# Kernel tuning notes

Hardware: AMD Instinct MI355X
Metric: run time of the kernel (lower is better)

Reference implementation:

```python
import jax, jax.numpy as jnp
import numpy as np

H, W = 512, 512
G = 8192
ALPHA_THRESH = 1.0 / 255.0        # meta_f32[0]
TRANS_THRESH = 1.0e-4             # meta_f32[1]
ALPHA_CAP = 0.99                  # meta_f32[6]
BG = jnp.zeros((3,), dtype=jnp.float32)  # config.background


def setup_inputs() -> dict:
    key = jax.random.key(0)
    ks = jax.random.split(key, 7)
    mx = jax.random.uniform(ks[0], (G,), minval=0.0, maxval=float(W))
    my = jax.random.uniform(ks[1], (G,), minval=0.0, maxval=float(H))
    means2d = jnp.stack([mx, my], axis=-1)
    # Build valid conics (inverse 2x2 covariances) from random rotation + scales
    theta = jax.random.uniform(ks[2], (G,), minval=0.0, maxval=2.0 * np.pi)
    s = jax.random.uniform(ks[3], (G, 2), minval=2.0, maxval=12.0)  # px stddevs
    ct, st = jnp.cos(theta), jnp.sin(theta)
    v1, v2 = s[:, 0] ** 2, s[:, 1] ** 2
    ca = ct * ct * v1 + st * st * v2
    cb = ct * st * (v1 - v2)
    cc = st * st * v1 + ct * ct * v2
    det = ca * cc - cb * cb
    conics = jnp.stack([cc / det, -cb / det, ca / det], axis=-1)  # [G,3] = (a,b,c)
    colors = jax.random.uniform(ks[4], (G, 3))
    opacities = jax.random.uniform(ks[5], (G,))
    depths = jax.random.uniform(ks[6], (G,), minval=0.1, maxval=100.0)
    return {"means2d": means2d, "conics": conics, "colors": colors,
            "opacities": opacities, "depths": depths}


def reference(means2d, conics, colors, opacities, depths):
    # Stable front-to-back depth sort (mirrors perm = argsort(depths, stable))
    perm = jnp.argsort(depths, stable=True)
    m = means2d[perm]
    cn = conics[perm]
    col = colors[perm]
    op = opacities[perm]
    a, b, c = cn[:, 0], cn[:, 1], cn[:, 2]
    px = jnp.arange(W, dtype=means2d.dtype) + 0.5  # pixel centers

    def row(y):
        py = y.astype(means2d.dtype) + 0.5
        dx = px[:, None] - m[None, :, 0]          # [W,G]
        dy = py - m[:, 1]                          # [G]
        sigma = 0.5 * (a * dx * dx + c * dy * dy) + b * dx * dy  # [W,G]
        alpha = jnp.minimum(ALPHA_CAP, op * jnp.exp(-sigma))
        alpha = jnp.where((sigma < 0) | (alpha < ALPHA_THRESH), 0.0, alpha)
        # exclusive cumulative transmittance along depth order
        Tprev = jnp.cumprod(1.0 - alpha, axis=-1)
        Tprev = jnp.concatenate([jnp.ones((W, 1), alpha.dtype), Tprev[:, :-1]], axis=-1)
        # early-termination: splats seen after T drops below threshold contribute 0
        wgt = alpha * Tprev * (Tprev >= TRANS_THRESH)  # [W,G]
        rgb = wgt @ col                                 # [W,3]
        t_rem = 1.0 - wgt.sum(axis=-1)                  # remaining transmittance
        return rgb + t_rem[:, None] * BG

    return jax.lax.map(row, jnp.arange(H))  # [H,W,3]
```

## Files before the change

kernel.cpp:

```cpp
#include <hip/hip_runtime.h>

#define G 8192
#define IMG_W 512
#define IMG_H 512
#define TILE 16
#define NTX (IMG_W / TILE)
#define NTY (IMG_H / TILE)
#define BLK 256
#define BLKB 64
#define CAP 1024
#define ALPHA_THRESH (1.0f/255.0f)
#define ALPHA_CAP 0.99f
#define TRANS_THRESH 1e-4f

__global__ __launch_bounds__(BLK)
void range_kernel(const float* __restrict__ means2d,
                  const float* __restrict__ conics,
                  const float* __restrict__ colors,
                  const float* __restrict__ opac,
                  unsigned int* __restrict__ ranges,
                  float* __restrict__ tbl)
{
    int g = blockIdx.x * BLK + threadIdx.x;
    if (g >= G) return;
    float op = opac[g];
    float a  = conics[3*g], b = conics[3*g+1], c = conics[3*g+2];
    float mx = means2d[2*g], my = means2d[2*g+1];
    float cr = colors[3*g], cg = colors[3*g+1], cb = colors[3*g+2];

    float4* t4 = (float4*)(tbl + (g << 4));
    t4[0] = make_float4(mx, my, 0.5f * a, b);
    t4[1] = make_float4(0.5f * c, op, cr, cg);
    t4[2] = make_float4(cb, 0.0f, 0.0f, 0.0f);

    unsigned int packed = 0xFFu;
    if (op * 255.0f >= 1.0f) {
        float smax = __logf(op * 255.0f);
        float det = fmaxf(a * c - b * b, 1e-12f);
        float rx = sqrtf(fmaxf(2.0f * smax * c / det, 0.0f)) * 1.0001f + 0.01f;
        float ry = sqrtf(fmaxf(2.0f * smax * a / det, 0.0f)) * 1.0001f + 0.01f;
        int txmin = (int)ceilf ((mx - rx - 15.5f) * 0.0625f);
        int txmax = (int)floorf((mx + rx -  0.5f) * 0.0625f);
        int tymin = (int)ceilf ((my - ry - 15.5f) * 0.0625f);
        int tymax = (int)floorf((my + ry -  0.5f) * 0.0625f);
        if (!(txmax < 0 || txmin > NTX-1 || tymax < 0 || tymin > NTY-1 ||
              txmin > txmax || tymin > tymax)) {
            txmin = max(txmin, 0); txmax = min(txmax, NTX-1);
            tymin = max(tymin, 0); tymax = min(tymax, NTY-1);
            packed = (unsigned)txmin | ((unsigned)txmax << 8)
                   | ((unsigned)tymin << 16) | ((unsigned)tymax << 24);
        }
    }
    ranges[g] = packed;
}

__device__ __forceinline__ int hitp(unsigned p, unsigned btx, unsigned bty)
{
    return (btx >= (p & 0xffu)) & (btx <= ((p >> 8) & 0xffu)) &
           (bty >= ((p >> 16) & 0xffu)) & (bty <= (p >> 24));
}

__global__ __launch_bounds__(BLK)
void tile_kernel(const unsigned int* __restrict__ ranges,
                 const float* __restrict__ depths,
                 const float* __restrict__ tbl,
                 float*       __restrict__ out)
{
    __shared__ __align__(16) unsigned short slist[CAP];
    __shared__ __align__(16) unsigned int fkeys[CAP + 8];
    __shared__ int woff[4];
    __shared__ __align__(16) float4 sq0[4][BLKB];
    __shared__ __align__(16) float4 sq1[4][BLKB];
    __shared__ __align__(16) float  sq2[4][BLKB];
    __shared__ float4 part[4][BLK];

    const int t = threadIdx.x;
    const int lane = t & 63, w = t >> 6;
    const unsigned btx = blockIdx.x, bty = blockIdx.y;

    const uint4* r4 = (const uint4*)ranges;
    const int wbase = w * (G / 4);
    uint4 rv[8];
    #pragma unroll
    for (int i = 0; i < 8; ++i)
        rv[i] = r4[(wbase >> 2) + i * 64 + lane];

    int cnt = 0;
    #pragma unroll
    for (int i = 0; i < 8; ++i)
        cnt += hitp(rv[i].x, btx, bty) + hitp(rv[i].y, btx, bty)
             + hitp(rv[i].z, btx, bty) + hitp(rv[i].w, btx, bty);
    #pragma unroll
    for (int d = 1; d < 64; d <<= 1) cnt += __shfl_xor(cnt, d);
    if (lane == 0) woff[w] = cnt;
    __syncthreads();

    int offs = 0;
    for (int ww = 0; ww < w; ++ww) offs += woff[ww];
    const int N = min(woff[0] + woff[1] + woff[2] + woff[3], CAP);

    const unsigned long long lt = (1ull << lane) - 1ull;
    #pragma unroll
    for (int i = 0; i < 8; ++i) {
        int gbase = wbase + i * 256 + lane * 4;
        int h0 = hitp(rv[i].x, btx, bty), h1 = hitp(rv[i].y, btx, bty);
        int h2 = hitp(rv[i].z, btx, bty), h3 = hitp(rv[i].w, btx, bty);
        unsigned long long m0 = __ballot(h0), m1 = __ballot(h1);
        unsigned long long m2 = __ballot(h2), m3 = __ballot(h3);
        int pos = offs + __popcll(m0 & lt) + __popcll(m1 & lt)
                       + __popcll(m2 & lt) + __popcll(m3 & lt);
        if (h0) { if (pos < CAP) slist[pos] = (unsigned short)(gbase    ); pos++; }
        if (h1) { if (pos < CAP) slist[pos] = (unsigned short)(gbase + 1); pos++; }
        if (h2) { if (pos < CAP) slist[pos] = (unsigned short)(gbase + 2); pos++; }
        if (h3) { if (pos < CAP) slist[pos] = (unsigned short)(gbase + 3); pos++; }
        offs += __popcll(m0) + __popcll(m1) + __popcll(m2) + __popcll(m3);
    }
    __syncthreads();

    unsigned short myidx[4]; unsigned int mykey[4]; int myr[4];
    #pragma unroll
    for (int m = 0; m < 4; ++m) {
        int i = t + m * BLK;
        if (i < N) {
            unsigned idx = slist[i];
            unsigned k = __float_as_uint(depths[idx]);
            myidx[m] = (unsigned short)idx; mykey[m] = k; fkeys[i] = k;
        }
    }
    if (t < 8) fkeys[N + t] = 0xFFFFFFFFu;
    __syncthreads();

    const uint4* fk4 = (const uint4*)fkeys;
    const int nj4 = (N + 3) >> 2;
    #pragma unroll
    for (int m = 0; m < 4; ++m) {
        int i = t + m * BLK;
        if (i < N) {
            unsigned ke = mykey[m]; int r = 0;
            for (int j4 = 0; j4 < nj4; ++j4) {
                uint4 kv = fk4[j4]; int j = j4 << 2;
                r += (int)((kv.x < ke) | ((kv.x == ke) & (j     < i)));
                r += (int)((kv.y < ke) | ((kv.y == ke) & (j + 1 < i)));
                r += (int)((kv.z < ke) | ((kv.z == ke) & (j + 2 < i)));
                r += (int)((kv.w < ke) | ((kv.w == ke) & (j + 3 < i)));
            }
            myr[m] = r;
        }
    }
    __syncthreads();
    #pragma unroll
    for (int m = 0; m < 4; ++m) {
        int i = t + m * BLK;
        if (i < N) slist[myr[m]] = myidx[m];
    }
    __syncthreads();

    const int csz = (N + 3) >> 2;
    const int cs = w * csz;
    const int ce = min(N, cs + csz);

    const float px  = (float)(btx * TILE + (lane & 15)) + 0.5f;
    const int   y0  = (lane >> 4) << 2;
    const float py0 = (float)(bty * TILE + y0) + 0.5f;
    const float py1 = py0 + 1.0f, py2 = py0 + 2.0f, py3 = py0 + 3.0f;

    float T0=1.f,T1=1.f,T2=1.f,T3=1.f;
    float ar0=0.f,ag0=0.f,ab0=0.f, ar1=0.f,ag1=0.f,ab1=0.f;
    float ar2=0.f,ag2=0.f,ab2=0.f, ar3=0.f,ag3=0.f,ab3=0.f;

    for (int base = cs; base < ce; base += BLKB) {
        int k = min(BLKB, ce - base);
        float4 v0 = make_float4(0.f,0.f,0.f,0.f);
        float4 v1 = make_float4(0.f,0.f,0.f,0.f);
        float  v2 = 0.f;
        if (lane < k) {
            int idx = slist[base + lane];
            const float4* b = (const float4*)(tbl + (idx << 4));
            v0 = b[0]; v1 = b[1]; v2 = ((const float*)b)[8];
        }
        sq0[w][lane] = v0; sq1[w][lane] = v1; sq2[w][lane] = v2;
        __threadfence_block();

        int k4 = (k + 3) & ~3;
        #pragma unroll 2
        for (int i = 0; i < k4; i += 4) {
            float4 blv = *(const float4*)&sq2[w][i];
            #pragma unroll
            for (int u = 0; u < 4; ++u) {
                float4 q0 = sq0[w][i + u];
                float4 q1 = sq1[w][i + u];
                float  bl = (u == 0) ? blv.x : (u == 1) ? blv.y
                          : (u == 2) ? blv.z : blv.w;
                float dx = px - q0.x;
                float dxdx = dx * dx;
                float dy0 = py0 - q0.y, dy1 = py1 - q0.y;
                float dy2 = py2 - q0.y, dy3 = py3 - q0.y;
                float sg0 = fmaf(q0.z, dxdx, fmaf(q1.x, dy0*dy0, q0.w*(dx*dy0)));
                float sg1 = fmaf(q0.z, dxdx, fmaf(q1.x, dy1*dy1, q0.w*(dx*dy1)));
                float sg2 = fmaf(q0.z, dxdx, fmaf(q1.x, dy2*dy2, q0.w*(dx*dy2)));
                float sg3 = fmaf(q0.z, dxdx, fmaf(q1.x, dy3*dy3, q0.w*(dx*dy3)));
                float al0 = q1.y * __expf(-sg0);
                float al1 = q1.y * __expf(-sg1);
                float al2 = q1.y * __expf(-sg2);
                float al3 = q1.y * __expf(-sg3);
                al0 = ((sg0 >= 0.f) && (al0 >= ALPHA_THRESH)) ? fminf(al0, ALPHA_CAP) : 0.f;
                al1 = ((sg1 >= 0.f) && (al1 >= ALPHA_THRESH)) ? fminf(al1, ALPHA_CAP) : 0.f;
                al2 = ((sg2 >= 0.f) && (al2 >= ALPHA_THRESH)) ? fminf(al2, ALPHA_CAP) : 0.f;
                al3 = ((sg3 >= 0.f) && (al3 >= ALPHA_THRESH)) ? fminf(al3, ALPHA_CAP) : 0.f;
                float w0 = al0*T0, w1 = al1*T1, w2 = al2*T2, w3 = al3*T3;
                ar0 = fmaf(w0, q1.z, ar0);  ar1 = fmaf(w1, q1.z, ar1);
                ar2 = fmaf(w2, q1.z, ar2);  ar3 = fmaf(w3, q1.z, ar3);
                ag0 = fmaf(w0, q1.w, ag0);  ag1 = fmaf(w1, q1.w, ag1);
                ag2 = fmaf(w2, q1.w, ag2);  ag3 = fmaf(w3, q1.w, ag3);
                ab0 = fmaf(w0, bl,   ab0);  ab1 = fmaf(w1, bl,   ab1);
                ab2 = fmaf(w2, bl,   ab2);  ab3 = fmaf(w3, bl,   ab3);
                T0 *= (1.f - al0);
                T1 *= (1.f - al1);
                T2 *= (1.f - al2);
                T3 *= (1.f - al3);
            }
        }
        if (__all((T0 < TRANS_THRESH) & (T1 < TRANS_THRESH) &
                  (T2 < TRANS_THRESH) & (T3 < TRANS_THRESH))) break;
    }

    {
        const int xl = lane & 15;
        part[w][(y0    ) * 16 + xl] = make_float4(ar0, ag0, ab0, T0);
        part[w][(y0 + 1) * 16 + xl] = make_float4(ar1, ag1, ab1, T1);
        part[w][(y0 + 2) * 16 + xl] = make_float4(ar2, ag2, ab2, T2);
        part[w][(y0 + 3) * 16 + xl] = make_float4(ar3, ag3, ab3, T3);
    }
    __syncthreads();

    float4 p0 = part[0][t], p1 = part[1][t], p2 = part[2][t], p3 = part[3][t];
    float r = p3.x, g = p3.y, b = p3.z;
    r = fmaf(p2.w, r, p2.x); g = fmaf(p2.w, g, p2.y); b = fmaf(p2.w, b, p2.z);
    r = fmaf(p1.w, r, p1.x); g = fmaf(p1.w, g, p1.y); b = fmaf(p1.w, b, p1.z);
    r = fmaf(p0.w, r, p0.x); g = fmaf(p0.w, g, p0.y); b = fmaf(p0.w, b, p0.z);

    const int X = (int)btx * TILE + (t & 15);
    const int Y = (int)bty * TILE + (t >> 4);
    const int o = (Y * IMG_W + X) * 3;
    out[o]     = r;
    out[o + 1] = g;
    out[o + 2] = b;
}

extern "C" void kernel_launch(void* const* d_in, const int* in_sizes, int n_in,
                              void* d_out, int out_size, void* d_ws, size_t ws_size,
                              hipStream_t stream)
{
    const float* means2d = (const float*)d_in[0];
    const float* conics  = (const float*)d_in[1];
    const float* colors  = (const float*)d_in[2];
    const float* opac    = (const float*)d_in[3];
    const float* depths  = (const float*)d_in[4];
    float* out = (float*)d_out;
    unsigned int* ranges = (unsigned int*)d_ws;
    float* tbl = (float*)((char*)d_ws + 32 * 1024);

    range_kernel<<<G / BLK, BLK, 0, stream>>>(means2d, conics, colors, opac,
                                              ranges, tbl);
    tile_kernel<<<dim3(NTX, NTY), dim3(BLK), 0, stream>>>(
        ranges, depths, tbl, out);
}
```

Measured before the change: 86.62 us.

## Cull splat-tile pairs with exact ellipse-rectangle test and per-tile bitmask

For splats whose bounding tile rectangle covers at most 32 tiles, the range kernel now tests each tile against the ellipse contour where alpha reaches the threshold, and stores a per-tile hit bitmask next to packed geometry in a uint2. Larger splats keep the plain bounding-box test. The tile kernel reads twice as much range data and decodes the mask, aiming to shrink per-tile splat lists and cut wasted exp/blend work. The sigma evaluation is also refactored into a Horner-style form that needs fewer multiplies. The trade-off is more range-kernel work, more range bytes read per tile block, and more registers for the 16 uint4 loads.

```diff
diff --git a/kernel.cpp b/kernel.cpp
--- a/kernel.cpp
+++ b/kernel.cpp
@@ -13,12 +13,44 @@
 #define ALPHA_CAP 0.99f
 #define TRANS_THRESH 1e-4f
 
+__device__ __forceinline__ bool ell_rect(float X0, float X1, float Y0, float Y1,
+                                         float a, float b, float c,
+                                         float det, float smaxt)
+{
+    if ((X0 <= 0.f) && (X1 >= 0.f) && (Y0 <= 0.f) && (Y1 >= 0.f)) return true;
+    #pragma unroll
+    for (int e = 0; e < 2; ++e) {
+        float xb = e ? X1 : X0;
+        float t = -b * xb;
+        bool lo = (t < Y0 * c);
+        bool in = !lo && (t <= Y1 * c);
+        if (in) { if (xb*xb*det <= 2.f*smaxt*c) return true; }
+        else {
+            float yc = lo ? Y0 : Y1;
+            if (0.5f*a*xb*xb + b*xb*yc + 0.5f*c*yc*yc <= smaxt) return true;
+        }
+    }
+    #pragma unroll
+    for (int e = 0; e < 2; ++e) {
+        float yb = e ? Y1 : Y0;
+        float t = -b * yb;
+        bool lo = (t < X0 * a);
+        bool in = !lo && (t <= X1 * a);
+        if (in) { if (yb*yb*det <= 2.f*smaxt*a) return true; }
+        else {
+            float xc = lo ? X0 : X1;
+            if (0.5f*a*xc*xc + b*xc*yb + 0.5f*c*yb*yb <= smaxt) return true;
+        }
+    }
+    return false;
+}
+
 __global__ __launch_bounds__(BLK)
 void range_kernel(const float* __restrict__ means2d,
                   const float* __restrict__ conics,
                   const float* __restrict__ colors,
                   const float* __restrict__ opac,
-                  unsigned int* __restrict__ ranges,
+                  uint2* __restrict__ ranges,
                   float* __restrict__ tbl)
 {
     int g = blockIdx.x * BLK + threadIdx.x;
@@ -33,7 +65,7 @@
     t4[1] = make_float4(0.5f * c, op, cr, cg);
     t4[2] = make_float4(cb, 0.0f, 0.0f, 0.0f);
 
-    unsigned int packed = 0xFFu;
+    unsigned geo = 0u, mask = 0u;
     if (op * 255.0f >= 1.0f) {
         float smax = __logf(op * 255.0f);
         float det = fmaxf(a * c - b * b, 1e-12f);
@@ -47,21 +79,48 @@
               txmin > txmax || tymin > tymax)) {
             txmin = max(txmin, 0); txmax = min(txmax, NTX-1);
             tymin = max(tymin, 0); tymax = min(tymax, NTY-1);
-            packed = (unsigned)txmin | ((unsigned)txmax << 8)
-                   | ((unsigned)tymin << 16) | ((unsigned)tymax << 24);
-        }
-    }
-    ranges[g] = packed;
-}
-
-__device__ __forceinline__ int hitp(unsigned p, unsigned btx, unsigned bty)
-{
-    return (btx >= (p & 0xffu)) & (btx <= ((p >> 8) & 0xffu)) &
-           (bty >= ((p >> 16) & 0xffu)) & (bty <= (p >> 24));
+            int wd = txmax - txmin + 1, ht = tymax - tymin + 1;
+            if (wd * ht > 32) {
+                geo = (unsigned)txmin | ((unsigned)tymin << 6)
+                    | ((unsigned)wd << 12) | ((unsigned)ht << 16) | (1u << 20);
+            } else {
+                float smaxt = smax * 1.0002f + 1e-3f;
+                unsigned m = 0u;
+                for (int tj = 0; tj < ht; ++tj) {
+                    float Y0 = (float)((tymin + tj) * TILE) + 0.5f - my - 0.01f;
+                    float Y1 = Y0 + 15.02f;
+                    for (int ti = 0; ti < wd; ++ti) {
+                        float X0 = (float)((txmin + ti) * TILE) + 0.5f - mx - 0.01f;
+                        float X1 = X0 + 15.02f;
+                        if (ell_rect(X0, X1, Y0, Y1, a, b, c, det, smaxt))
+                            m |= 1u << (tj * wd + ti);
+                    }
+                }
+                if (m) {
+                    geo = (unsigned)txmin | ((unsigned)tymin << 6)
+                        | ((unsigned)wd << 12) | ((unsigned)ht << 16);
+                    mask = m;
+                }
+            }
+        }
+    }
+    ranges[g] = make_uint2(geo, mask);
+}
+
+__device__ __forceinline__ int hitp2(unsigned geo, unsigned mask,
+                                     unsigned btx, unsigned bty)
+{
+    unsigned txm = geo & 63u, tym = (geo >> 6) & 63u;
+    unsigned wd  = (geo >> 12) & 15u, ht = (geo >> 16) & 15u;
+    unsigned dxt = btx - txm, dyt = bty - tym;
+    int inr = (dxt < wd) & (dyt < ht);
+    unsigned bi = dyt * wd + dxt;
+    int mb = (geo >> 20) ? 1 : (int)((mask >> (bi & 31u)) & 1u);
+    return inr & mb;
 }
 
 __global__ __launch_bounds__(BLK)
-void tile_kernel(const unsigned int* __restrict__ ranges,
+void tile_kernel(const uint2* __restrict__ ranges,
                  const float* __restrict__ depths,
                  const float* __restrict__ tbl,
                  float*       __restrict__ out)
@@ -80,16 +139,16 @@
 
     const uint4* r4 = (const uint4*)ranges;
     const int wbase = w * (G / 4);
-    uint4 rv[8];
-    #pragma unroll
-    for (int i = 0; i < 8; ++i)
-        rv[i] = r4[(wbase >> 2) + i * 64 + lane];
+    uint4 rv[16];
+    #pragma unroll
+    for (int i = 0; i < 16; ++i)
+        rv[i] = r4[(wbase >> 1) + i * 64 + lane];
 
     int cnt = 0;
     #pragma unroll
-    for (int i = 0; i < 8; ++i)
-        cnt += hitp(rv[i].x, btx, bty) + hitp(rv[i].y, btx, bty)
-             + hitp(rv[i].z, btx, bty) + hitp(rv[i].w, btx, bty);
+    for (int i = 0; i < 16; ++i)
+        cnt += hitp2(rv[i].x, rv[i].y, btx, bty)
+             + hitp2(rv[i].z, rv[i].w, btx, bty);
     #pragma unroll
     for (int d = 1; d < 64; d <<= 1) cnt += __shfl_xor(cnt, d);
     if (lane == 0) woff[w] = cnt;
@@ -101,19 +160,15 @@
 
     const unsigned long long lt = (1ull << lane) - 1ull;
     #pragma unroll
-    for (int i = 0; i < 8; ++i) {
-        int gbase = wbase + i * 256 + lane * 4;
-        int h0 = hitp(rv[i].x, btx, bty), h1 = hitp(rv[i].y, btx, bty);
-        int h2 = hitp(rv[i].z, btx, bty), h3 = hitp(rv[i].w, btx, bty);
+    for (int i = 0; i < 16; ++i) {
+        int gbase = wbase + i * 128 + lane * 2;
+        int h0 = hitp2(rv[i].x, rv[i].y, btx, bty);
+        int h1 = hitp2(rv[i].z, rv[i].w, btx, bty);
         unsigned long long m0 = __ballot(h0), m1 = __ballot(h1);
-        unsigned long long m2 = __ballot(h2), m3 = __ballot(h3);
-        int pos = offs + __popcll(m0 & lt) + __popcll(m1 & lt)
-                       + __popcll(m2 & lt) + __popcll(m3 & lt);
+        int pos = offs + __popcll(m0 & lt) + __popcll(m1 & lt);
         if (h0) { if (pos < CAP) slist[pos] = (unsigned short)(gbase    ); pos++; }
-        if (h1) { if (pos < CAP) slist[pos] = (unsigned short)(gbase + 1); pos++; }
-        if (h2) { if (pos < CAP) slist[pos] = (unsigned short)(gbase + 2); pos++; }
-        if (h3) { if (pos < CAP) slist[pos] = (unsigned short)(gbase + 3); pos++; }
-        offs += __popcll(m0) + __popcll(m1) + __popcll(m2) + __popcll(m3);
+        if (h1) { if (pos < CAP) slist[pos] = (unsigned short)(gbase + 1); }
+        offs += __popcll(m0) + __popcll(m1);
     }
     __syncthreads();
 
@@ -192,13 +247,14 @@
                 float  bl = (u == 0) ? blv.x : (u == 1) ? blv.y
                           : (u == 2) ? blv.z : blv.w;
                 float dx = px - q0.x;
-                float dxdx = dx * dx;
+                float A  = q0.z * (dx * dx);
+                float Bx = q0.w * dx;
                 float dy0 = py0 - q0.y, dy1 = py1 - q0.y;
                 float dy2 = py2 - q0.y, dy3 = py3 - q0.y;
-                float sg0 = fmaf(q0.z, dxdx, fmaf(q1.x, dy0*dy0, q0.w*(dx*dy0)));
-                float sg1 = fmaf(q0.z, dxdx, fmaf(q1.x, dy1*dy1, q0.w*(dx*dy1)));
-                float sg2 = fmaf(q0.z, dxdx, fmaf(q1.x, dy2*dy2, q0.w*(dx*dy2)));
-                float sg3 = fmaf(q0.z, dxdx, fmaf(q1.x, dy3*dy3, q0.w*(dx*dy3)));
+                float sg0 = fmaf(dy0, fmaf(q1.x, dy0, Bx), A);
+                float sg1 = fmaf(dy1, fmaf(q1.x, dy1, Bx), A);
+                float sg2 = fmaf(dy2, fmaf(q1.x, dy2, Bx), A);
+                float sg3 = fmaf(dy3, fmaf(q1.x, dy3, Bx), A);
                 float al0 = q1.y * __expf(-sg0);
                 float al1 = q1.y * __expf(-sg1);
                 float al2 = q1.y * __expf(-sg2);
@@ -257,8 +313,8 @@
     const float* opac    = (const float*)d_in[3];
     const float* depths  = (const float*)d_in[4];
     float* out = (float*)d_out;
-    unsigned int* ranges = (unsigned int*)d_ws;
-    float* tbl = (float*)((char*)d_ws + 32 * 1024);
+    uint2* ranges = (uint2*)d_ws;
+    float* tbl = (float*)((char*)d_ws + 64 * 1024);
 
     range_kernel<<<G / BLK, BLK, 0, stream>>>(means2d, conics, colors, opac,
                                               ranges, tbl);
```

Result: slower. 108.4 us (+25.1%).

## Split tile kernel into separate sort and single-wave compositing kernels

Applied to the files above, without the earlier changes.

Splits the fused per-tile kernel into a sort kernel, which writes each tile's depth-sorted splat list and count to workspace, and a compositing kernel launched with one 64-thread wave per tile that walks the whole list sequentially. This drops the four-wave split of the list and the shared-memory partial-transmittance merge, and gives the compositing loop a fully serial early-termination check. The cost is an extra launch, a global round trip of the sorted lists, and fewer threads per tile during compositing, which may lower latency hiding.

```diff
diff --git a/kernel.cpp b/kernel.cpp
--- a/kernel.cpp
+++ b/kernel.cpp
@@ -6,12 +6,16 @@
 #define TILE 16
 #define NTX (IMG_W / TILE)
 #define NTY (IMG_H / TILE)
+#define NTILES (NTX * NTY)
 #define BLK 256
-#define BLKB 64
 #define CAP 1024
 #define ALPHA_THRESH (1.0f/255.0f)
 #define ALPHA_CAP 0.99f
 #define TRANS_THRESH 1e-4f
+
+#define OFF_TBL   32768
+#define OFF_LIST  (OFF_TBL + G*64)
+#define OFF_N     (OFF_LIST + NTILES*CAP*2)
 
 __global__ __launch_bounds__(BLK)
 void range_kernel(const float* __restrict__ means2d,
@@ -61,22 +65,19 @@
 }
 
 __global__ __launch_bounds__(BLK)
-void tile_kernel(const unsigned int* __restrict__ ranges,
+void sort_kernel(const unsigned int* __restrict__ ranges,
                  const float* __restrict__ depths,
-                 const float* __restrict__ tbl,
-                 float*       __restrict__ out)
+                 unsigned short* __restrict__ lists,
+                 int* __restrict__ tile_n)
 {
     __shared__ __align__(16) unsigned short slist[CAP];
     __shared__ __align__(16) unsigned int fkeys[CAP + 8];
     __shared__ int woff[4];
-    __shared__ __align__(16) float4 sq0[4][BLKB];
-    __shared__ __align__(16) float4 sq1[4][BLKB];
-    __shared__ __align__(16) float  sq2[4][BLKB];
-    __shared__ float4 part[4][BLK];
 
     const int t = threadIdx.x;
     const int lane = t & 63, w = t >> 6;
     const unsigned btx = blockIdx.x, bty = blockIdx.y;
+    const int tile = (int)bty * NTX + (int)btx;
 
     const uint4* r4 = (const uint4*)ranges;
     const int wbase = w * (G / 4);
@@ -155,42 +156,54 @@
     }
     __syncthreads();
 
-    const int csz = (N + 3) >> 2;
-    const int cs = w * csz;
-    const int ce = min(N, cs + csz);
-
-    const float px  = (float)(btx * TILE + (lane & 15)) + 0.5f;
+    for (int i = t; i < N; i += BLK) lists[tile * CAP + i] = slist[i];
+    if (t == 0) tile_n[tile] = N;
+}
+
+__global__ __launch_bounds__(64)
+void comp_kernel(const unsigned short* __restrict__ lists,
+                 const int* __restrict__ tile_n,
+                 const float* __restrict__ tbl,
+                 float* __restrict__ out)
+{
+    __shared__ __align__(16) float4 sq0[64];
+    __shared__ __align__(16) float4 sq1[64];
+    __shared__ __align__(16) float  sq2[64];
+
+    const int tile = blockIdx.x;
+    const int lane = threadIdx.x;
+    const int N = tile_n[tile];
+    const int tx = tile & (NTX - 1), ty = tile >> 5;
+
+    const float px  = (float)(tx * TILE + (lane & 15)) + 0.5f;
     const int   y0  = (lane >> 4) << 2;
-    const float py0 = (float)(bty * TILE + y0) + 0.5f;
+    const float py0 = (float)(ty * TILE + y0) + 0.5f;
     const float py1 = py0 + 1.0f, py2 = py0 + 2.0f, py3 = py0 + 3.0f;
 
     float T0=1.f,T1=1.f,T2=1.f,T3=1.f;
     float ar0=0.f,ag0=0.f,ab0=0.f, ar1=0.f,ag1=0.f,ab1=0.f;
     float ar2=0.f,ag2=0.f,ab2=0.f, ar3=0.f,ag3=0.f,ab3=0.f;
 
-    for (int base = cs; base < ce; base += BLKB) {
-        int k = min(BLKB, ce - base);
+    for (int base = 0; base < N; base += 64) {
+        int k = min(64, N - base);
         float4 v0 = make_float4(0.f,0.f,0.f,0.f);
         float4 v1 = make_float4(0.f,0.f,0.f,0.f);
         float  v2 = 0.f;
         if (lane < k) {
-            int idx = slist[base + lane];
+            int idx = lists[tile * CAP + base + lane];
             const float4* b = (const float4*)(tbl + (idx << 4));
             v0 = b[0]; v1 = b[1]; v2 = ((const float*)b)[8];
         }
-        sq0[w][lane] = v0; sq1[w][lane] = v1; sq2[w][lane] = v2;
+        sq0[lane] = v0; sq1[lane] = v1; sq2[lane] = v2;
         __threadfence_block();
 
         int k4 = (k + 3) & ~3;
-        #pragma unroll 2
         for (int i = 0; i < k4; i += 4) {
-            float4 blv = *(const float4*)&sq2[w][i];
             #pragma unroll
             for (int u = 0; u < 4; ++u) {
-                float4 q0 = sq0[w][i + u];
-                float4 q1 = sq1[w][i + u];
-                float  bl = (u == 0) ? blv.x : (u == 1) ? blv.y
-                          : (u == 2) ? blv.z : blv.w;
+                float4 q0 = sq0[i + u];
+                float4 q1 = sq1[i + u];
+                float  bl = sq2[i + u];
                 float dx = px - q0.x;
                 float dxdx = dx * dx;
                 float dy0 = py0 - q0.y, dy1 = py1 - q0.y;
@@ -224,27 +237,20 @@
                   (T2 < TRANS_THRESH) & (T3 < TRANS_THRESH))) break;
     }
 
-    {
-        const int xl = lane & 15;
-        part[w][(y0    ) * 16 + xl] = make_float4(ar0, ag0, ab0, T0);
-        part[w][(y0 + 1) * 16 + xl] = make_float4(ar1, ag1, ab1, T1);
-        part[w][(y0 + 2) * 16 + xl] = make_float4(ar2, ag2, ab2, T2);
-        part[w][(y0 + 3) * 16 + xl] = make_float4(ar3, ag3, ab3, T3);
-    }
-    __syncthreads();
-
-    float4 p0 = part[0][t], p1 = part[1][t], p2 = part[2][t], p3 = part[3][t];
-    float r = p3.x, g = p3.y, b = p3.z;
-    r = fmaf(p2.w, r, p2.x); g = fmaf(p2.w, g, p2.y); b = fmaf(p2.w, b, p2.z);
-    r = fmaf(p1.w, r, p1.x); g = fmaf(p1.w, g, p1.y); b = fmaf(p1.w, b, p1.z);
-    r = fmaf(p0.w, r, p0.x); g = fmaf(p0.w, g, p0.y); b = fmaf(p0.w, b, p0.z);
-
-    const int X = (int)btx * TILE + (t & 15);
-    const int Y = (int)bty * TILE + (t >> 4);
-    const int o = (Y * IMG_W + X) * 3;
-    out[o]     = r;
-    out[o + 1] = g;
-    out[o + 2] = b;
+    const int X = tx * TILE + (lane & 15);
+    const int o0 = (((ty * TILE + y0) * IMG_W) + X) * 3;
+    out[o0]               = ar0;
+    out[o0 + 1]           = ag0;
+    out[o0 + 2]           = ab0;
+    out[o0 + 3*IMG_W]     = ar1;
+    out[o0 + 3*IMG_W + 1] = ag1;
+    out[o0 + 3*IMG_W + 2] = ab1;
+    out[o0 + 6*IMG_W]     = ar2;
+    out[o0 + 6*IMG_W + 1] = ag2;
+    out[o0 + 6*IMG_W + 2] = ab2;
+    out[o0 + 9*IMG_W]     = ar3;
+    out[o0 + 9*IMG_W + 1] = ag3;
+    out[o0 + 9*IMG_W + 2] = ab3;
 }
 
 extern "C" void kernel_launch(void* const* d_in, const int* in_sizes, int n_in,
@@ -257,11 +263,15 @@
     const float* opac    = (const float*)d_in[3];
     const float* depths  = (const float*)d_in[4];
     float* out = (float*)d_out;
-    unsigned int* ranges = (unsigned int*)d_ws;
-    float* tbl = (float*)((char*)d_ws + 32 * 1024);
+
+    unsigned int*   ranges = (unsigned int*)d_ws;
+    float*          tbl    = (float*)((char*)d_ws + OFF_TBL);
+    unsigned short* lists  = (unsigned short*)((char*)d_ws + OFF_LIST);
+    int*            tile_n = (int*)((char*)d_ws + OFF_N);
 
     range_kernel<<<G / BLK, BLK, 0, stream>>>(means2d, conics, colors, opac,
                                               ranges, tbl);
-    tile_kernel<<<dim3(NTX, NTY), dim3(BLK), 0, stream>>>(
-        ranges, depths, tbl, out);
-}
+    sort_kernel<<<dim3(NTX, NTY), BLK, 0, stream>>>(ranges, depths,
+                                                    lists, tile_n);
+    comp_kernel<<<NTILES, 64, 0, stream>>>(lists, tile_n, tbl, out);
+}
```

Measured after the change: 97.37 us. 12.4% more time.

## Globally depth-rank gaussians once and drop per-tile rank sort

Applied to the files above, without the earlier changes.

Adds a rank kernel that computes each gaussian's global stable depth rank by counting comparisons against all 8192 depth keys held in shared memory. The range kernel then scatters the table and range entries into depth order, so each tile's ballot compaction already yields a sorted list and the per-tile O(N^2) rank sort is removed. This costs an extra launch and 8192x8192 comparisons globally, plus a 32KB shared buffer per block, in exchange for removing the per-tile sort work across 1024 tiles.

```diff
diff --git a/kernel.cpp b/kernel.cpp
--- a/kernel.cpp
+++ b/kernel.cpp
@@ -13,11 +13,54 @@
 #define ALPHA_CAP 0.99f
 #define TRANS_THRESH 1e-4f
 
+#define OFF_RANK  32768
+#define OFF_TBL   65536
+
+__global__ __launch_bounds__(BLK)
+void rank_kernel(const float* __restrict__ depths, int* __restrict__ rank)
+{
+    __shared__ __align__(16) unsigned keys[G];
+    __shared__ int acc[8][32];
+
+    const int t = threadIdx.x;
+    const uint4* d4 = (const uint4*)depths;
+    #pragma unroll
+    for (int i = 0; i < 8; ++i)
+        ((uint4*)keys)[t + i * BLK] = d4[t + i * BLK];
+    __syncthreads();
+
+    const int gi = t & 31;
+    const int sl = t >> 5;
+    const int g  = blockIdx.x * 32 + gi;
+    const unsigned kg = keys[g];
+
+    const uint4* k4 = (const uint4*)keys;
+    const int jb = sl * 256;
+    int r = 0;
+    for (int j4 = 0; j4 < 256; ++j4) {
+        uint4 kv = k4[jb + j4];
+        int j = (jb + j4) << 2;
+        r += (int)((kv.x < kg) | ((kv.x == kg) & (j     < g)));
+        r += (int)((kv.y < kg) | ((kv.y == kg) & (j + 1 < g)));
+        r += (int)((kv.z < kg) | ((kv.z == kg) & (j + 2 < g)));
+        r += (int)((kv.w < kg) | ((kv.w == kg) & (j + 3 < g)));
+    }
+    acc[sl][gi] = r;
+    __syncthreads();
+    if (t < 32) {
+        int s = 0;
+        #pragma unroll
+        for (int i = 0; i < 8; ++i) s += acc[i][t];
+        rank[blockIdx.x * 32 + t] = s;
+    }
+}
+
 __global__ __launch_bounds__(BLK)
 void range_kernel(const float* __restrict__ means2d,
                   const float* __restrict__ conics,
                   const float* __restrict__ colors,
                   const float* __restrict__ opac,
+                  const int* __restrict__ rank,
                   unsigned int* __restrict__ ranges,
                   float* __restrict__ tbl)
 {
@@ -27,8 +70,9 @@
     float a  = conics[3*g], b = conics[3*g+1], c = conics[3*g+2];
     float mx = means2d[2*g], my = means2d[2*g+1];
     float cr = colors[3*g], cg = colors[3*g+1], cb = colors[3*g+2];
-
-    float4* t4 = (float4*)(tbl + (g << 4));
+    const int rk = rank[g];
+
+    float4* t4 = (float4*)(tbl + (rk << 4));
     t4[0] = make_float4(mx, my, 0.5f * a, b);
     t4[1] = make_float4(0.5f * c, op, cr, cg);
     t4[2] = make_float4(cb, 0.0f, 0.0f, 0.0f);
@@ -51,7 +95,7 @@
                    | ((unsigned)tymin << 16) | ((unsigned)tymax << 24);
         }
     }
-    ranges[g] = packed;
+    ranges[rk] = packed;
 }
 
 __device__ __forceinline__ int hitp(unsigned p, unsigned btx, unsigned bty)
@@ -62,12 +106,10 @@
 
 __global__ __launch_bounds__(BLK)
 void tile_kernel(const unsigned int* __restrict__ ranges,
-                 const float* __restrict__ depths,
                  const float* __restrict__ tbl,
                  float*       __restrict__ out)
 {
     __shared__ __align__(16) unsigned short slist[CAP];
-    __shared__ __align__(16) unsigned int fkeys[CAP + 8];
     __shared__ int woff[4];
     __shared__ __align__(16) float4 sq0[4][BLKB];
     __shared__ __align__(16) float4 sq1[4][BLKB];
@@ -114,44 +156,6 @@
         if (h2) { if (pos < CAP) slist[pos] = (unsigned short)(gbase + 2); pos++; }
         if (h3) { if (pos < CAP) slist[pos] = (unsigned short)(gbase + 3); pos++; }
         offs += __popcll(m0) + __popcll(m1) + __popcll(m2) + __popcll(m3);
-    }
-    __syncthreads();
-
-    unsigned short myidx[4]; unsigned int mykey[4]; int myr[4];
-    #pragma unroll
-    for (int m = 0; m < 4; ++m) {
-        int i = t + m * BLK;
-        if (i < N) {
-            unsigned idx = slist[i];
-            unsigned k = __float_as_uint(depths[idx]);
-            myidx[m] = (unsigned short)idx; mykey[m] = k; fkeys[i] = k;
-        }
-    }
-    if (t < 8) fkeys[N + t] = 0xFFFFFFFFu;
-    __syncthreads();
-
-    const uint4* fk4 = (const uint4*)fkeys;
-    const int nj4 = (N + 3) >> 2;
-    #pragma unroll
-    for (int m = 0; m < 4; ++m) {
-        int i = t + m * BLK;
-        if (i < N) {
-            unsigned ke = mykey[m]; int r = 0;
-            for (int j4 = 0; j4 < nj4; ++j4) {
-                uint4 kv = fk4[j4]; int j = j4 << 2;
-                r += (int)((kv.x < ke) | ((kv.x == ke) & (j     < i)));
-                r += (int)((kv.y < ke) | ((kv.y == ke) & (j + 1 < i)));
-                r += (int)((kv.z < ke) | ((kv.z == ke) & (j + 2 < i)));
-                r += (int)((kv.w < ke) | ((kv.w == ke) & (j + 3 < i)));
-            }
-            myr[m] = r;
-        }
-    }
-    __syncthreads();
-    #pragma unroll
-    for (int m = 0; m < 4; ++m) {
-        int i = t + m * BLK;
-        if (i < N) slist[myr[m]] = myidx[m];
     }
     __syncthreads();
 
@@ -257,11 +261,13 @@
     const float* opac    = (const float*)d_in[3];
     const float* depths  = (const float*)d_in[4];
     float* out = (float*)d_out;
+
     unsigned int* ranges = (unsigned int*)d_ws;
-    float* tbl = (float*)((char*)d_ws + 32 * 1024);
-
+    int*          rankb  = (int*)((char*)d_ws + OFF_RANK);
+    float*        tbl    = (float*)((char*)d_ws + OFF_TBL);
+
+    rank_kernel<<<G / 32, BLK, 0, stream>>>(depths, rankb);
     range_kernel<<<G / BLK, BLK, 0, stream>>>(means2d, conics, colors, opac,
-                                              ranges, tbl);
-    tile_kernel<<<dim3(NTX, NTY), dim3(BLK), 0, stream>>>(
-        ranges, depths, tbl, out);
-}
+                                              rankb, ranges, tbl);
+    tile_kernel<<<dim3(NTX, NTY), dim3(BLK), 0, stream>>>(ranges, tbl, out);
+}
```

Result: slower. 111.4 us (+28.6%).
